# Optimization experiments

Measured on AMD Instinct MI355X. Metric: run time of the kernel, lower is better.

Reference implementation:

```python
import jax, jax.numpy as jnp
import numpy as np

SCALAR_DIM = 452          # 2 + 6 + (110+1)*4
GRID_C, GRID_H, GRID_W = 2, 32, 18
GRID_FLAT = GRID_C * GRID_H * GRID_W  # 1152
OBS_DIM = SCALAR_DIM + GRID_FLAT      # 1604
CNN_OUT, SC_OUT, HID, N_ACT = 128, 64, 128, 2305
CNN_FLAT = 64 * 8 * 5                 # 32x18 -> 16x9 -> 8x5
T, B = 256, 128


def setup_inputs() -> dict:
    key = jax.random.key(0)
    ks = jax.random.split(key, 24)
    p = lambda k, shape: jax.random.normal(k, shape, jnp.float32) * 0.02
    return dict(
        obs_seq=jax.random.uniform(ks[0], (T, B, OBS_DIM), jnp.float32),
        h0=jnp.zeros((1, B, HID), jnp.float32),
        c0=jnp.zeros((1, B, HID), jnp.float32),
        done_mask=jax.random.randint(ks[1], (T, B), 0, 2) > 0,
        conv1_w=p(ks[2], (32, GRID_C, 3, 3)), conv1_b=jnp.zeros((32,), jnp.float32),
        conv2_w=p(ks[3], (64, 32, 3, 3)),     conv2_b=jnp.zeros((64,), jnp.float32),
        conv3_w=p(ks[4], (64, 64, 3, 3)),     conv3_b=jnp.zeros((64,), jnp.float32),
        fc_w=p(ks[5], (CNN_OUT, CNN_FLAT)),   fc_b=jnp.zeros((CNN_OUT,), jnp.float32),
        s1_w=p(ks[6], (64, SCALAR_DIM)),      s1_b=jnp.zeros((64,), jnp.float32),
        s2_w=p(ks[7], (SC_OUT, 64)),          s2_b=jnp.zeros((SC_OUT,), jnp.float32),
        w_ih=p(ks[8], (4 * HID, CNN_OUT + SC_OUT)),
        w_hh=p(ks[9], (4 * HID, HID)),
        b_ih=jnp.zeros((4 * HID,), jnp.float32),
        b_hh=jnp.zeros((4 * HID,), jnp.float32),
        pol_w=p(ks[10], (N_ACT, HID)), pol_b=jnp.zeros((N_ACT,), jnp.float32),
        val_w=p(ks[11], (1, HID)),     val_b=jnp.zeros((1,), jnp.float32),
    )


def _conv(x, w, b, stride):
    y = jax.lax.conv_general_dilated(
        x, w, (stride, stride), ((1, 1), (1, 1)),
        dimension_numbers=("NCHW", "OIHW", "NCHW"))
    return y + b[None, :, None, None]


def reference(obs_seq, h0, c0, done_mask,
              conv1_w, conv1_b, conv2_w, conv2_b, conv3_w, conv3_b,
              fc_w, fc_b, s1_w, s1_b, s2_w, s2_b,
              w_ih, w_hh, b_ih, b_hh, pol_w, pol_b, val_w, val_b):
    Tt, Bb, _ = obs_seq.shape
    flat = obs_seq.reshape(Tt * Bb, -1)
    scalars = flat[:, :SCALAR_DIM]
    grid = flat[:, SCALAR_DIM:SCALAR_DIM + GRID_FLAT].reshape(-1, GRID_C, GRID_H, GRID_W)

    # CNN encoder
    x = jax.nn.relu(_conv(grid, conv1_w, conv1_b, 1))
    x = jax.nn.relu(_conv(x, conv2_w, conv2_b, 2))
    x = jax.nn.relu(_conv(x, conv3_w, conv3_b, 2))
    cnn = jax.nn.relu(x.reshape(x.shape[0], -1) @ fc_w.T + fc_b)

    # scalar MLP
    sc = jax.nn.relu(jax.nn.relu(scalars @ s1_w.T + s1_b) @ s2_w.T + s2_b)

    emb = jnp.concatenate([cnn, sc], axis=-1).reshape(Tt, Bb, -1)  # (T,B,192)

    # episode-reset mask applied BEFORE each step (for t>0, from done[t-1])
    keep = jnp.concatenate(
        [jnp.ones((1, Bb), jnp.float32),
         1.0 - done_mask[:-1].astype(jnp.float32)], axis=0)[..., None]  # (T,B,1)

    def step(carry, inp):
        h, c = carry
        x_t, k_t = inp
        h = h * k_t
        c = c * k_t
        g = x_t @ w_ih.T + h @ w_hh.T + b_ih + b_hh
        i, f, gg, o = jnp.split(g, 4, axis=-1)  # torch gate order i,f,g,o
        c = jax.nn.sigmoid(f) * c + jax.nn.sigmoid(i) * jnp.tanh(gg)
        h = jax.nn.sigmoid(o) * jnp.tanh(c)
        return (h, c), h

    (h_f, c_f), outs = jax.lax.scan(step, (h0[0], c0[0]), (emb, keep))

    logits = outs @ pol_w.T + pol_b   # (T,B,n_actions)
    values = outs @ val_w.T + val_b   # (T,B,1)
    return logits, values, h_f[None], c_f[None]
```

## Files before the change

kernel.cpp:

```cpp
#include <hip/hip_runtime.h>


typedef __attribute__((ext_vector_type(8))) short v8s;
typedef __attribute__((ext_vector_type(4))) float v4f;
typedef __attribute__((ext_vector_type(4))) unsigned int v4u;

#define DEV static __device__ __forceinline__

DEV unsigned int cvtpk(float lo, float hi){
  unsigned int d;
  asm("v_cvt_pk_bf16_f32 %0, %1, %2" : "=v"(d) : "v"(lo), "v"(hi));
  return d;
}
DEV unsigned short f2bf(float x){ return (unsigned short)(cvtpk(x, x) & 0xffffu); }
DEV float bf2f(unsigned short h){ return __uint_as_float(((unsigned int)h) << 16); }
DEV unsigned int pkbf(float a, float b){ return cvtpk(a, b); }
DEV v4f MFMA(v8s a, v8s b, v4f c){ return __builtin_amdgcn_mfma_f32_16x16x32_bf16(a, b, c, 0, 0, 0); }
DEV v4f vzero(){ v4f z = {0.f, 0.f, 0.f, 0.f}; return z; }
DEV float relu(float x){ return x > 0.f ? x : 0.f; }
DEV float sigm(float x){ return 1.0f / (1.0f + __expf(-x)); }
DEV float tanhfast(float x){
  x = fminf(15.0f, fmaxf(-15.0f, x));
  float e = __expf(2.0f * x);
  return (e - 1.0f) / (e + 1.0f);
}
DEV uint2 pack4(v4f a, float4 b){
  return make_uint2(cvtpk(relu(a[0]+b.x), relu(a[1]+b.y)),
                    cvtpk(relu(a[2]+b.z), relu(a[3]+b.w)));
}
union U8S { v4u u4; v8s s8; };

__global__ __launch_bounds__(256) void pack_all(
    const float* __restrict__ c1w, const float* __restrict__ c2w,
    const float* __restrict__ c3w, const float* __restrict__ fcw,
    const float* __restrict__ s1w, const float* __restrict__ s2w,
    const float* __restrict__ wih, const float* __restrict__ whh,
    const float* __restrict__ pw,
    unsigned short* __restrict__ w1p, unsigned short* __restrict__ w2p,
    unsigned short* __restrict__ w3p, unsigned short* __restrict__ fcp,
    unsigned short* __restrict__ s1p, unsigned short* __restrict__ s2p,
    unsigned short* __restrict__ lsp, unsigned short* __restrict__ pop){
  int b = blockIdx.x;
  const float *src, *src2 = nullptr; unsigned short* dst;
  int N, K, KS, CI, mode, rel;
  if      (b < 4)   { src=c1w; dst=w1p; N=32;  K=24;  KS=1;  CI=2;  mode=4; rel=b; }
  else if (b < 76)  { src=c2w; dst=w2p; N=64;  K=288; KS=9;  CI=32; mode=1; rel=b-4; }
  else if (b < 220) { src=c3w; dst=w3p; N=64;  K=576; KS=18; CI=64; mode=1; rel=b-76; }
  else if (b < 1500){ src=fcw; dst=fcp; N=128; K=2560;KS=80; CI=0;  mode=2; rel=b-220; }
  else if (b < 1620){ src=s1w; dst=s1p; N=64;  K=452; KS=15; CI=0;  mode=0; rel=b-1500; }
  else if (b < 1636){ src=s2w; dst=s2p; N=64;  K=64;  KS=2;  CI=0;  mode=0; rel=b-1620; }
  else if (b < 2276){ src=wih; src2=whh; dst=lsp; N=512; K=320; KS=10; CI=0; mode=3; rel=b-1636; }
  else              { src=pw;  dst=pop; N=2305;K=128; KS=4;  CI=0;  mode=0; rel=b-2276; }
  int idx = rel * 256 + threadIdx.x;
  int e  = idx & 7;
  int l  = (idx >> 3) & 63;
  int fs = idx >> 9;
  int ks = fs % KS;
  int nt = fs / KS;
  int n = nt * 16 + (l & 15);
  int k = ks * 32 + (l >> 4) * 8 + e;
  float v = 0.f;
  if (n < N && k < K){
    if (mode == 0)      v = src[n * K + k];
    else if (mode == 1){ int p9 = k / CI, ci = k - p9 * CI; v = src[(n * CI + ci) * 9 + p9]; }
    else if (mode == 2){ int pos = k >> 6, ci = k & 63;     v = src[n * 2560 + ci * 40 + pos]; }
    else if (mode == 3) v = (k < 192) ? src[n * 192 + k] : src2[n * 128 + (k - 192)];
    else { int dy = k >> 3, r = k & 7, dx = r >> 1, ci = r & 1;
           if (dx < 3) v = src[(n * 2 + ci) * 9 + dy * 3 + dx]; }
  }
  dst[idx] = f2bf(v);
}

__global__ __launch_bounds__(512) void bias_kernel(const float* __restrict__ bih,
    const float* __restrict__ bhh, float* __restrict__ bias512){
  int t = threadIdx.x;
  if (t < 512) bias512[t] = bih[t] + bhh[t];
}

__global__ __launch_bounds__(256) void mlp_kernel(const float* __restrict__ obs,
    const unsigned short* __restrict__ s1p, const unsigned short* __restrict__ s2p,
    const float* __restrict__ s1b, const float* __restrict__ s2b,
    unsigned short* __restrict__ emb){
  __shared__ __align__(16) unsigned short xl[32 * 488];
  __shared__ __align__(16) unsigned short h1[32 * 72];
  int tid = threadIdx.x, w = tid >> 6, l = tid & 63, i = l & 15, u = l >> 4;
  long s0 = (long)blockIdx.x * 32;
  for (int idx = tid; idx < 32 * 113; idx += 256){
    int r = idx / 113, q = idx - r * 113;
    float4 v = *(const float4*)&obs[(s0 + r) * 1604 + q * 4];
    *(uint2*)&xl[r * 488 + q * 4] = make_uint2(pkbf(v.x, v.y), pkbf(v.z, v.w));
  }
  for (int idx = tid; idx < 32 * 28; idx += 256){
    int r = idx / 28, k = 452 + (idx - r * 28);
    xl[r * 488 + k] = 0;
  }
  __syncthreads();
  v4f acc0 = vzero(), acc1 = vzero();
  const v8s* F1 = (const v8s*)s1p;
  #pragma unroll
  for (int ks = 0; ks < 15; ++ks){
    v8s bb = F1[(w * 15 + ks) * 64 + l];
    v8s aa0 = *(const v8s*)&xl[(0 * 16 + i) * 488 + ks * 32 + u * 8];
    v8s aa1 = *(const v8s*)&xl[(1 * 16 + i) * 488 + ks * 32 + u * 8];
    acc0 = MFMA(aa0, bb, acc0);
    acc1 = MFMA(aa1, bb, acc1);
  }
  float b1 = s1b[w * 16 + i];
  #pragma unroll
  for (int r = 0; r < 4; ++r){
    float v0 = relu(acc0[r] + b1);
    float v1 = relu(acc1[r] + b1);
    h1[(u * 4 + r) * 72 + w * 16 + i] = f2bf(v0);
    h1[(16 + u * 4 + r) * 72 + w * 16 + i] = f2bf(v1);
  }
  __syncthreads();
  v4f a20 = vzero(), a21 = vzero();
  const v8s* F2 = (const v8s*)s2p;
  #pragma unroll
  for (int ks = 0; ks < 2; ++ks){
    v8s bb = F2[(w * 2 + ks) * 64 + l];
    v8s aa0 = *(const v8s*)&h1[(0 * 16 + i) * 72 + ks * 32 + u * 8];
    v8s aa1 = *(const v8s*)&h1[(1 * 16 + i) * 72 + ks * 32 + u * 8];
    a20 = MFMA(aa0, bb, a20);
    a21 = MFMA(aa1, bb, a21);
  }
  float b2 = s2b[w * 16 + i];
  #pragma unroll
  for (int r = 0; r < 4; ++r){
    float v0 = relu(a20[r] + b2);
    float v1 = relu(a21[r] + b2);
    emb[(s0 + u * 4 + r) * 192 + 128 + w * 16 + i] = f2bf(v0);
    emb[(s0 + 16 + u * 4 + r) * 192 + 128 + w * 16 + i] = f2bf(v1);
  }
}

#define ACT1o 0
#define ACT2o 43520
#define GRIDo 68864
#define SWZ(p) ((((p) >> 1) & 7) << 4)

__global__ __launch_bounds__(512, 2) void conv_kernel(const float* __restrict__ obs,
    const unsigned short* __restrict__ w1p, const unsigned short* __restrict__ w2p,
    const unsigned short* __restrict__ w3p,
    const float* __restrict__ b1v, const float* __restrict__ b2v, const float* __restrict__ b3v,
    unsigned short* __restrict__ act3g){
  __shared__ __align__(16) char lds[74496];
  int tid = threadIdx.x, w = tid >> 6, l = tid & 63, i = l & 15, u = l >> 4;
  int nh2 = w & 1, pt2 = w >> 1;
  int cp = w & 1, t3 = w >> 1;
  const v8s* W1 = (const v8s*)w1p;
  const v8s* W2 = (const v8s*)w2p;
  const v8s* W3 = (const v8s*)w3p;
  v8s w1f0 = W1[l], w1f1 = W1[64 + l];
  float4 bc1a = *(const float4*)&b1v[u * 4];
  float4 bc1b = *(const float4*)&b1v[16 + u * 4];
  float4 bc2a = *(const float4*)&b2v[nh2 * 32 + u * 4];
  float4 bc2b = *(const float4*)&b2v[nh2 * 32 + 16 + u * 4];
  float4 bc3a = *(const float4*)&b3v[cp * 32 + u * 4];
  float4 bc3b = *(const float4*)&b3v[cp * 32 + 16 + u * 4];
  for (int idx = tid; idx < 18624; idx += 512) *(unsigned int*)(lds + idx * 4) = 0u;
  int soff[4];
  #pragma unroll
  for (int j = 0; j < 4; ++j){
    int p = tid * 4 + j, r = p / 18, c = p - r * 18;
    soff[j] = ((r + 1) * 20 + (c + 1)) * 4;
  }
  __syncthreads();
  long sbase = (long)blockIdx.x * 64;
  if (tid < 144){
    const float4* gp = (const float4*)(obs + sbase * 1604 + 452);
    float4 a = gp[tid], b = gp[tid + 144];
    *(unsigned int*)(lds + GRIDo + soff[0]) = pkbf(a.x, b.x);
    *(unsigned int*)(lds + GRIDo + soff[1]) = pkbf(a.y, b.y);
    *(unsigned int*)(lds + GRIDo + soff[2]) = pkbf(a.z, b.z);
    *(unsigned int*)(lds + GRIDo + soff[3]) = pkbf(a.w, b.w);
  }
  __syncthreads();

  int praw3 = t3 * 16 + i;
  int pos3 = praw3 > 39 ? 39 : praw3;
  int oh3 = pos3 / 5, ow3 = pos3 - oh3 * 5;
  int pr3 = (2 * oh3) * 11 + 2 * ow3;

  for (int it = 0; it < 64; ++it){
    long s = sbase + it;
    int gbo = GRIDo + (it & 1) * 2816;
    int z2; asm("s_mov_b32 %0, 0" : "=s"(z2) : "s"(it));
    v8s w2f[2][9];
    #pragma unroll
    for (int jj = 0; jj < 2; ++jj)
      #pragma unroll
      for (int t = 0; t < 9; ++t) w2f[jj][t] = W2[((nh2 * 2 + jj) * 9 + t) * 64 + l + z2];
    float4 pa, pb; bool pf = (it < 63) && (tid < 144);
    if (pf){
      const float4* gp = (const float4*)(obs + (s + 1) * 1604 + 452);
      pa = gp[tid]; pb = gp[tid + 144];
    }
    #pragma unroll
    for (int k = 0; k < 5; ++k){
      int ntl = w + 8 * k;
      if (ntl < 36){
        int pos = ntl * 16 + i;
        int oh = pos / 18, ow = pos - oh * 18;
        int glin = gbo + ((oh + u) * 20 + ow) * 4;
        U8S gv;
        gv.u4.x = *(const unsigned int*)(lds + glin);
        gv.u4.y = *(const unsigned int*)(lds + glin + 4);
        gv.u4.z = *(const unsigned int*)(lds + glin + 8);
        gv.u4.w = *(const unsigned int*)(lds + glin + 12);
        v4f a0 = MFMA(w1f0, gv.s8, vzero());
        v4f a1 = MFMA(w1f1, gv.s8, vzero());
        int p1 = (oh + 1) * 20 + (ow + 1);
        int sA = SWZ(p1);
        *(uint2*)(lds + ACT1o + ((p1 * 64 + u * 8) ^ sA))      = pack4(a0, bc1a);
        *(uint2*)(lds + ACT1o + ((p1 * 64 + 32 + u * 8) ^ sA)) = pack4(a1, bc1b);
      }
    }
    __syncthreads();
    #pragma unroll
    for (int kk = 0; kk < 3; ++kk){
      int ntl = pt2 + 4 * kk;
      if (ntl < 9){
        int pos2 = ntl * 16 + i;
        int oh = pos2 / 9, ow = pos2 - oh * 9;
        int pr0 = (2 * oh) * 20 + 2 * ow;
        v4f a0 = vzero(), a1 = vzero();
        #pragma unroll
        for (int dy = 0; dy < 3; ++dy)
          #pragma unroll
          for (int dx = 0; dx < 3; ++dx){
            int p = pr0 + dy * 20 + dx;
            int byte = (p * 64 + u * 16) ^ SWZ(p);
            v8s bf = *(const v8s*)(lds + ACT1o + byte);
            a0 = MFMA(w2f[0][dy * 3 + dx], bf, a0);
            a1 = MFMA(w2f[1][dy * 3 + dx], bf, a1);
          }
        int p2 = (oh + 1) * 11 + (ow + 1);
        int sB = SWZ(p2);
        *(uint2*)(lds + ACT2o + ((p2 * 128 + nh2 * 64 + u * 8) ^ sB))      = pack4(a0, bc2a);
        *(uint2*)(lds + ACT2o + ((p2 * 128 + nh2 * 64 + 32 + u * 8) ^ sB)) = pack4(a1, bc2b);
      }
    }
    if (pf){
      int gbn = GRIDo + ((it + 1) & 1) * 2816;
      *(unsigned int*)(lds + gbn + soff[0]) = pkbf(pa.x, pb.x);
      *(unsigned int*)(lds + gbn + soff[1]) = pkbf(pa.y, pb.y);
      *(unsigned int*)(lds + gbn + soff[2]) = pkbf(pa.z, pb.z);
      *(unsigned int*)(lds + gbn + soff[3]) = pkbf(pa.w, pb.w);
    }
    __syncthreads();
    if (w < 6){
      int z3; asm("s_mov_b32 %0, 0" : "=s"(z3) : "s"(it));
      v4f c30 = vzero(), c31 = vzero();
      #pragma unroll
      for (int ksh = 0; ksh < 2; ++ksh){
        const int t0 = ksh * 5, tc = ksh ? 4 : 5;
        v8s w3q[2][5][2];
        #pragma unroll
        for (int j = 0; j < 2; ++j)
          #pragma unroll
          for (int tt = 0; tt < 5; ++tt){
            if (tt < tc){
              #pragma unroll
              for (int h = 0; h < 2; ++h)
                w3q[j][tt][h] = W3[((2 * cp + j) * 18 + 2 * (t0 + tt) + h) * 64 + l + z3];
            }
          }
        #pragma unroll
        for (int tt = 0; tt < 5; ++tt){
          if (tt < tc){
            int tap = t0 + tt, dy = tap / 3, dx = tap - dy * 3;
            int dpp = dy * 11 + dx;
            #pragma unroll
            for (int h = 0; h < 2; ++h){
              int p = pr3 + dpp;
              int byte = (p * 128 + h * 64 + u * 16) ^ SWZ(p);
              v8s bf = *(const v8s*)(lds + ACT2o + byte);
              c30 = MFMA(w3q[0][tt][h], bf, c30);
              c31 = MFMA(w3q[1][tt][h], bf, c31);
            }
          }
        }
      }
      if (praw3 < 40){
        unsigned short* dg = act3g + s * 2560;
        *(uint2*)(dg + praw3 * 64 + cp * 32 + u * 4)      = pack4(c30, bc3a);
        *(uint2*)(dg + praw3 * 64 + cp * 32 + 16 + u * 4) = pack4(c31, bc3b);
      }
    }
  }
}

__global__ __launch_bounds__(256) void fc_kernel(const unsigned short* __restrict__ act3g,
    const unsigned short* __restrict__ fcp, const float* __restrict__ fcb,
    unsigned short* __restrict__ emb){
  __shared__ __align__(16) unsigned short al[64 * 264];
  int tid = threadIdx.x, w = tid >> 6, l = tid & 63, i = l & 15, u = l >> 4;
  long s0 = (long)blockIdx.x * 64;
  v4f acc[4][2];
  #pragma unroll
  for (int mt = 0; mt < 4; ++mt){ acc[mt][0] = vzero(); acc[mt][1] = vzero(); }
  const v8s* F = (const v8s*)fcp;
  for (int kc = 0; kc < 10; ++kc){
    __syncthreads();
    for (int idx = tid; idx < 64 * 32; idx += 256){
      int r = idx >> 5, q = idx & 31;
      *(v8s*)&al[r * 264 + q * 8] = *(const v8s*)&act3g[(s0 + r) * 2560 + kc * 256 + q * 8];
    }
    __syncthreads();
    #pragma unroll
    for (int ksl = 0; ksl < 8; ++ksl){
      v8s b0 = F[((w * 2 + 0) * 80 + kc * 8 + ksl) * 64 + l];
      v8s b1 = F[((w * 2 + 1) * 80 + kc * 8 + ksl) * 64 + l];
      #pragma unroll
      for (int mt = 0; mt < 4; ++mt){
        v8s aa = *(const v8s*)&al[(mt * 16 + i) * 264 + ksl * 32 + u * 8];
        acc[mt][0] = MFMA(aa, b0, acc[mt][0]);
        acc[mt][1] = MFMA(aa, b1, acc[mt][1]);
      }
    }
  }
  float fb0 = fcb[(w * 2) * 16 + i], fb1 = fcb[(w * 2 + 1) * 16 + i];
  #pragma unroll
  for (int mt = 0; mt < 4; ++mt)
    #pragma unroll
    for (int r = 0; r < 4; ++r){
      float v0 = relu(acc[mt][0][r] + fb0);
      float v1 = relu(acc[mt][1][r] + fb1);
      emb[(s0 + mt * 16 + u * 4 + r) * 192 + (w * 2) * 16 + i] = f2bf(v0);
      emb[(s0 + mt * 16 + u * 4 + r) * 192 + (w * 2 + 1) * 16 + i] = f2bf(v1);
    }
}

__global__ __launch_bounds__(256) void segprep_kernel(const void* __restrict__ dmask,
    unsigned int* __restrict__ segs, int4* __restrict__ gtab, int* __restrict__ meta){
  __shared__ int cnt[257], off[257], place[257];
  __shared__ int notInt;
  int tid = threadIdx.x;
  for (int idx = tid; idx < 257; idx += 256){ cnt[idx] = 0; place[idx] = 0; }
  if (tid == 0) notInt = 0;
  __syncthreads();
  const unsigned char* p8 = (const unsigned char*)dmask;
  int nz = 0;
  for (int idx = tid; idx < 2048; idx += 256)
    if (p8[idx * 4 + 1] | p8[idx * 4 + 2] | p8[idx * 4 + 3]) nz = 1;
  if (nz) notInt = 1;
  __syncthreads();
  bool m32 = (notInt == 0);
  const int* p32 = (const int*)dmask;
  if (tid < 128){
    int b = tid, ts = 0;
    for (int t = 0; t < 256; ++t){
      bool d = (t == 255) ? true : (m32 ? (p32[t * 128 + b] != 0) : (p8[t * 128 + b] != 0));
      if (d){ atomicAdd(&cnt[t - ts + 1], 1); ts = t + 1; }
    }
  }
  __syncthreads();
  if (tid == 0){
    int acc = 0;
    for (int len = 1; len <= 256; ++len){ off[len] = acc; acc += cnt[len]; }
    int G = 0;
    for (int len = 1; len <= 256; ++len){
      int c = cnt[len], g = 0;
      while (c > 0){
        int take = c < 32 ? c : 32;
        gtab[G] = make_int4(len, off[len] + g * 32, take, 0);
        ++G; c -= 32; ++g;
      }
    }
    meta[0] = G;
  }
  __syncthreads();
  if (tid < 128){
    int b = tid, ts = 0;
    for (int t = 0; t < 256; ++t){
      bool d = (t == 255) ? true : (m32 ? (p32[t * 128 + b] != 0) : (p8[t * 128 + b] != 0));
      if (d){
        int len = t - ts + 1;
        int slot = off[len] + atomicAdd(&place[len], 1);
        segs[slot] = (unsigned int)(b | (ts << 8));
        ts = t + 1;
      }
    }
  }
}

__global__ __launch_bounds__(512) void lstm_kernel(
    const unsigned short* __restrict__ emb, const unsigned short* __restrict__ lstmp,
    const float* __restrict__ bias512,
    const float* __restrict__ h0, const float* __restrict__ c0,
    const unsigned int* __restrict__ segs, const int4* __restrict__ gtab,
    const int* __restrict__ meta,
    unsigned short* __restrict__ outsb, float* __restrict__ hf, float* __restrict__ cf){
  int grp = blockIdx.x;
  if (grp >= meta[0]) return;
  int4 gd = gtab[grp];
  int len = gd.x, base = gd.y, nseg = gd.z;
  __shared__ __align__(16) unsigned short hbuf[2][32 * 136];
  __shared__ int sb[32], st[32];
  int tid = threadIdx.x, w = tid >> 6, l = tid & 63, i = l & 15, u = l >> 4;
  if (tid < 32){
    unsigned int sv = segs[base + (tid < nseg ? tid : 0)];
    sb[tid] = (int)(sv & 127u);
    st[tid] = (int)((sv >> 8) & 255u);
  }
  __syncthreads();
  int j = w * 16 + i;
  float cst[2][4];
  #pragma unroll
  for (int mt = 0; mt < 2; ++mt)
    #pragma unroll
    for (int r = 0; r < 4; ++r){
      int slot = mt * 16 + u * 4 + r;
      float cv = 0.f, hv = 0.f;
      if (st[slot] == 0){ cv = c0[sb[slot] * 128 + j]; hv = h0[sb[slot] * 128 + j]; }
      cst[mt][r] = cv;
      hbuf[0][slot * 136 + j] = f2bf(hv);
    }
  float bi = bias512[j], bff = bias512[128 + j], bg = bias512[256 + j], bo = bias512[384 + j];
  int bA0 = sb[i], tA0 = st[i];
  int bA1 = sb[16 + i], tA1 = st[16 + i];
  __syncthreads();
  const v8s* LP = (const v8s*)lstmp;
  for (int step = 0; step < len; ++step){
    int pb = step & 1;
    v4f gi0 = vzero(), gi1 = vzero(), gf0 = vzero(), gf1 = vzero();
    v4f gg0 = vzero(), gg1 = vzero(), go0 = vzero(), go1 = vzero();
    #pragma unroll
    for (int ks = 0; ks < 10; ++ks){
      v8s a0, a1;
      if (ks < 6){
        a0 = *(const v8s*)&emb[((long)(tA0 + step) * 128 + bA0) * 192 + ks * 32 + u * 8];
        a1 = *(const v8s*)&emb[((long)(tA1 + step) * 128 + bA1) * 192 + ks * 32 + u * 8];
      } else {
        int koff = (ks - 6) * 32 + u * 8;
        a0 = *(const v8s*)&hbuf[pb][i * 136 + koff];
        a1 = *(const v8s*)&hbuf[pb][(16 + i) * 136 + koff];
      }
      v8s b_i = LP[((w) * 10 + ks) * 64 + l];
      v8s b_f = LP[((w + 8) * 10 + ks) * 64 + l];
      v8s b_g = LP[((w + 16) * 10 + ks) * 64 + l];
      v8s b_o = LP[((w + 24) * 10 + ks) * 64 + l];
      gi0 = MFMA(a0, b_i, gi0); gi1 = MFMA(a1, b_i, gi1);
      gf0 = MFMA(a0, b_f, gf0); gf1 = MFMA(a1, b_f, gf1);
      gg0 = MFMA(a0, b_g, gg0); gg1 = MFMA(a1, b_g, gg1);
      go0 = MFMA(a0, b_o, go0); go1 = MFMA(a1, b_o, go1);
    }
    #pragma unroll
    for (int mt = 0; mt < 2; ++mt)
      #pragma unroll
      for (int r = 0; r < 4; ++r){
        int slot = mt * 16 + u * 4 + r;
        float giv = mt ? gi1[r] : gi0[r];
        float gfv = mt ? gf1[r] : gf0[r];
        float ggv = mt ? gg1[r] : gg0[r];
        float gov = mt ? go1[r] : go0[r];
        float iv = sigm(giv + bi);
        float fv = sigm(gfv + bff);
        float gv = tanhfast(ggv + bg);
        float ov = sigm(gov + bo);
        float cv = fv * cst[mt][r] + iv * gv;
        cst[mt][r] = cv;
        float hv = ov * tanhfast(cv);
        unsigned short hb = f2bf(hv);
        hbuf[pb ^ 1][slot * 136 + j] = hb;
        if (slot < nseg){
          outsb[((long)(st[slot] + step) * 128 + sb[slot]) * 128 + j] = hb;
          if (st[slot] + len == 256 && step == len - 1){
            hf[sb[slot] * 128 + j] = hv;
            cf[sb[slot] * 128 + j] = cv;
          }
        }
      }
    __syncthreads();
  }
}

__global__ __launch_bounds__(256) void heads_kernel(const unsigned short* __restrict__ outsb,
    const unsigned short* __restrict__ polp, const float* __restrict__ polb,
    const float* __restrict__ vw, const float* __restrict__ vb,
    float* __restrict__ logits, float* __restrict__ values){
  __shared__ __align__(16) unsigned short al[64 * 136];
  int tid = threadIdx.x, w = tid >> 6, l = tid & 63, i = l & 15, u = l >> 4;
  long s0 = (long)blockIdx.x * 64;
  for (int idx = tid; idx < 64 * 16; idx += 256){
    int r = idx >> 4, q = idx & 15;
    *(v8s*)&al[r * 136 + q * 8] = *(const v8s*)&outsb[(s0 + r) * 128 + q * 8];
  }
  __syncthreads();
  v8s af[4][4];
  #pragma unroll
  for (int mt = 0; mt < 4; ++mt)
    #pragma unroll
    for (int ks = 0; ks < 4; ++ks)
      af[mt][ks] = *(const v8s*)&al[(mt * 16 + i) * 136 + ks * 32 + u * 8];
  const v8s* P = (const v8s*)polp;
  for (int nt = w; nt < 145; nt += 4){
    v4f acc[4];
    #pragma unroll
    for (int mt = 0; mt < 4; ++mt) acc[mt] = vzero();
    #pragma unroll
    for (int ks = 0; ks < 4; ++ks){
      v8s bb = P[(nt * 4 + ks) * 64 + l];
      #pragma unroll
      for (int mt = 0; mt < 4; ++mt) acc[mt] = MFMA(af[mt][ks], bb, acc[mt]);
    }
    int n = nt * 16 + i;
    if (n < 2305){
      float pbv = polb[n];
      #pragma unroll
      for (int mt = 0; mt < 4; ++mt)
        #pragma unroll
        for (int r = 0; r < 4; ++r)
          logits[(s0 + mt * 16 + u * 4 + r) * 2305 + n] = acc[mt][r] + pbv;
    }
  }
  float vacc = 0.f;
  #pragma unroll
  for (int g = 0; g < 4; ++g){
    float4 vA = *(const float4*)&vw[g * 32 + u * 8];
    float4 vB = *(const float4*)&vw[g * 32 + u * 8 + 4];
    v8s xv = *(const v8s*)&al[(w * 16 + i) * 136 + g * 32 + u * 8];
    vacc += bf2f((unsigned short)xv[0]) * vA.x + bf2f((unsigned short)xv[1]) * vA.y
          + bf2f((unsigned short)xv[2]) * vA.z + bf2f((unsigned short)xv[3]) * vA.w
          + bf2f((unsigned short)xv[4]) * vB.x + bf2f((unsigned short)xv[5]) * vB.y
          + bf2f((unsigned short)xv[6]) * vB.z + bf2f((unsigned short)xv[7]) * vB.w;
  }
  vacc += __shfl_xor(vacc, 16);
  vacc += __shfl_xor(vacc, 32);
  if (u == 0) values[s0 + w * 16 + i] = vacc + vb[0];
}

extern "C" void kernel_launch(void* const* d_in, const int* in_sizes, int n_in,
                              void* d_out, int out_size, void* d_ws, size_t ws_size,
                              hipStream_t stream){
  (void)in_sizes; (void)n_in; (void)out_size; (void)ws_size;
  const float* obs = (const float*)d_in[0];
  const float* h0  = (const float*)d_in[1];
  const float* c0  = (const float*)d_in[2];
  const void*  dm  = d_in[3];
  const float* c1w = (const float*)d_in[4];  const float* c1b = (const float*)d_in[5];
  const float* c2w = (const float*)d_in[6];  const float* c2b = (const float*)d_in[7];
  const float* c3w = (const float*)d_in[8];  const float* c3b = (const float*)d_in[9];
  const float* fcw = (const float*)d_in[10]; const float* fcb = (const float*)d_in[11];
  const float* s1w = (const float*)d_in[12]; const float* s1b = (const float*)d_in[13];
  const float* s2w = (const float*)d_in[14]; const float* s2b = (const float*)d_in[15];
  const float* wih = (const float*)d_in[16]; const float* whh = (const float*)d_in[17];
  const float* bih = (const float*)d_in[18]; const float* bhh = (const float*)d_in[19];
  const float* pw  = (const float*)d_in[20]; const float* pb  = (const float*)d_in[21];
  const float* vw  = (const float*)d_in[22]; const float* vb  = (const float*)d_in[23];

  char* ws = (char*)d_ws;
  size_t off = 0;
  auto take = [&](size_t sz)->char*{
    char* p = ws + off; off = (off + sz + 255) & ~(size_t)255; return p;
  };
  unsigned short* emb    = (unsigned short*)take(32768UL * 192 * 2);
  unsigned short* outsb  = (unsigned short*)take(32768UL * 128 * 2);
  unsigned short* w1p    = (unsigned short*)take(1024UL * 2);
  unsigned short* w2p    = (unsigned short*)take(18432UL * 2);
  unsigned short* w3p    = (unsigned short*)take(36864UL * 2);
  unsigned short* fcp    = (unsigned short*)take(327680UL * 2);
  unsigned short* s1p    = (unsigned short*)take(30720UL * 2);
  unsigned short* s2p    = (unsigned short*)take(4096UL * 2);
  unsigned short* lsp    = (unsigned short*)take(163840UL * 2);
  unsigned short* pop    = (unsigned short*)take(296960UL * 2);
  float*          b512   = (float*)take(512UL * 4);
  unsigned int*   segs   = (unsigned int*)take(32768UL * 4);
  int4*           gtab   = (int4*)take(1280UL * 16);
  int*            meta   = (int*)take(256);

  float* outp   = (float*)d_out;
  float* logits = outp;
  float* values = outp + 75530240L;
  float* hf     = outp + 75563008L;
  float* cf     = outp + 75579392L;
  unsigned short* act3g = (unsigned short*)d_out;

  dim3 b256(256), b512t(512);
  pack_all<<<dim3(3436), b256, 0, stream>>>(c1w, c2w, c3w, fcw, s1w, s2w, wih, whh, pw,
                                            w1p, w2p, w3p, fcp, s1p, s2p, lsp, pop);
  bias_kernel<<<dim3(1), b512t, 0, stream>>>(bih, bhh, b512);
  segprep_kernel<<<dim3(1), b256, 0, stream>>>(dm, segs, gtab, meta);
  mlp_kernel<<<dim3(1024), b256, 0, stream>>>(obs, s1p, s2p, s1b, s2b, emb);
  conv_kernel<<<dim3(512), b512t, 0, stream>>>(obs, w1p, w2p, w3p, c1b, c2b, c3b, act3g);
  fc_kernel<<<dim3(512), b256, 0, stream>>>(act3g, fcp, fcb, emb);
  lstm_kernel<<<dim3(1280), b512t, 0, stream>>>(emb, lsp, b512, h0, c0, segs, gtab, meta,
                                                outsb, hf, cf);
  heads_kernel<<<dim3(512), b256, 0, stream>>>(outsb, pop, pb, vw, vb, logits, values);
}
```

Measured before the change: 1.209 ms.

## Repartition conv2/conv3 work so each wave owns one 16-channel tile

Conv2 and conv3 waves are remapped so each wave handles a single 16-output-channel tile across several position tiles, instead of two channel tiles over fewer positions. All 8 waves now take part in conv3, where before only 6 did; waves 0-3 also pick up the partial third position tile. Each wave loads half as many weight fragments into registers, which eases register pressure. The cost is more LDS reads of activations per MFMA, since each B fragment now feeds one MFMA rather than two, and the conv3 load is uneven across waves.

```diff
diff --git a/kernel.cpp b/kernel.cpp
--- a/kernel.cpp
+++ b/kernel.cpp
@@ -146,18 +146,16 @@
     unsigned short* __restrict__ act3g){
   __shared__ __align__(16) char lds[74496];
   int tid = threadIdx.x, w = tid >> 6, l = tid & 63, i = l & 15, u = l >> 4;
-  int nh2 = w & 1, pt2 = w >> 1;
-  int cp = w & 1, t3 = w >> 1;
+  int ct = w & 3;
+  int ph = w >> 2;
   const v8s* W1 = (const v8s*)w1p;
   const v8s* W2 = (const v8s*)w2p;
   const v8s* W3 = (const v8s*)w3p;
   v8s w1f0 = W1[l], w1f1 = W1[64 + l];
   float4 bc1a = *(const float4*)&b1v[u * 4];
   float4 bc1b = *(const float4*)&b1v[16 + u * 4];
-  float4 bc2a = *(const float4*)&b2v[nh2 * 32 + u * 4];
-  float4 bc2b = *(const float4*)&b2v[nh2 * 32 + 16 + u * 4];
-  float4 bc3a = *(const float4*)&b3v[cp * 32 + u * 4];
-  float4 bc3b = *(const float4*)&b3v[cp * 32 + 16 + u * 4];
+  float4 bc2  = *(const float4*)&b2v[ct * 16 + u * 4];
+  float4 bc3  = *(const float4*)&b3v[ct * 16 + u * 4];
   for (int idx = tid; idx < 18624; idx += 512) *(unsigned int*)(lds + idx * 4) = 0u;
   int soff[4];
   #pragma unroll
@@ -177,20 +175,22 @@
   }
   __syncthreads();
 
-  int praw3 = t3 * 16 + i;
-  int pos3 = praw3 > 39 ? 39 : praw3;
-  int oh3 = pos3 / 5, ow3 = pos3 - oh3 * 5;
+  int praw3 = ph * 16 + i;
+  int oh3 = praw3 / 5, ow3 = praw3 - oh3 * 5;
   int pr3 = (2 * oh3) * 11 + 2 * ow3;
+  int praw3s = 32 + i;
+  int pos3s = praw3s > 39 ? 39 : praw3s;
+  int oh3s = pos3s / 5, ow3s = pos3s - oh3s * 5;
+  int pr3s = (2 * oh3s) * 11 + 2 * ow3s;
+  bool small3 = (w < 4);
 
   for (int it = 0; it < 64; ++it){
     long s = sbase + it;
     int gbo = GRIDo + (it & 1) * 2816;
     int z2; asm("s_mov_b32 %0, 0" : "=s"(z2) : "s"(it));
-    v8s w2f[2][9];
-    #pragma unroll
-    for (int jj = 0; jj < 2; ++jj)
-      #pragma unroll
-      for (int t = 0; t < 9; ++t) w2f[jj][t] = W2[((nh2 * 2 + jj) * 9 + t) * 64 + l + z2];
+    v8s w2f[9];
+    #pragma unroll
+    for (int t = 0; t < 9; ++t) w2f[t] = W2[(ct * 9 + t) * 64 + l + z2];
     float4 pa, pb; bool pf = (it < 63) && (tid < 144);
     if (pf){
       const float4* gp = (const float4*)(obs + (s + 1) * 1604 + 452);
@@ -218,13 +218,13 @@
     }
     __syncthreads();
     #pragma unroll
-    for (int kk = 0; kk < 3; ++kk){
-      int ntl = pt2 + 4 * kk;
+    for (int kk = 0; kk < 5; ++kk){
+      int ntl = ph + 2 * kk;
       if (ntl < 9){
         int pos2 = ntl * 16 + i;
         int oh = pos2 / 9, ow = pos2 - oh * 9;
         int pr0 = (2 * oh) * 20 + 2 * ow;
-        v4f a0 = vzero(), a1 = vzero();
+        v4f a = vzero();
         #pragma unroll
         for (int dy = 0; dy < 3; ++dy)
           #pragma unroll
@@ -232,13 +232,10 @@
             int p = pr0 + dy * 20 + dx;
             int byte = (p * 64 + u * 16) ^ SWZ(p);
             v8s bf = *(const v8s*)(lds + ACT1o + byte);
-            a0 = MFMA(w2f[0][dy * 3 + dx], bf, a0);
-            a1 = MFMA(w2f[1][dy * 3 + dx], bf, a1);
+            a = MFMA(w2f[dy * 3 + dx], bf, a);
           }
         int p2 = (oh + 1) * 11 + (ow + 1);
-        int sB = SWZ(p2);
-        *(uint2*)(lds + ACT2o + ((p2 * 128 + nh2 * 64 + u * 8) ^ sB))      = pack4(a0, bc2a);
-        *(uint2*)(lds + ACT2o + ((p2 * 128 + nh2 * 64 + 32 + u * 8) ^ sB)) = pack4(a1, bc2b);
+        *(uint2*)(lds + ACT2o + ((p2 * 128 + ct * 32 + u * 8) ^ SWZ(p2))) = pack4(a, bc2);
       }
     }
     if (pf){
@@ -249,44 +246,37 @@
       *(unsigned int*)(lds + gbn + soff[3]) = pkbf(pa.w, pb.w);
     }
     __syncthreads();
-    if (w < 6){
+    {
       int z3; asm("s_mov_b32 %0, 0" : "=s"(z3) : "s"(it));
-      v4f c30 = vzero(), c31 = vzero();
+      v4f c3 = vzero(), c3s = vzero();
       #pragma unroll
       for (int ksh = 0; ksh < 2; ++ksh){
-        const int t0 = ksh * 5, tc = ksh ? 4 : 5;
-        v8s w3q[2][5][2];
+        v8s w3h[9];
         #pragma unroll
-        for (int j = 0; j < 2; ++j)
-          #pragma unroll
-          for (int tt = 0; tt < 5; ++tt){
-            if (tt < tc){
-              #pragma unroll
-              for (int h = 0; h < 2; ++h)
-                w3q[j][tt][h] = W3[((2 * cp + j) * 18 + 2 * (t0 + tt) + h) * 64 + l + z3];
-            }
+        for (int t = 0; t < 9; ++t) w3h[t] = W3[(ct * 18 + ksh * 9 + t) * 64 + l + z3];
+        #pragma unroll
+        for (int t = 0; t < 9; ++t){
+          int ks = ksh * 9 + t, tap = ks >> 1, h = ks & 1;
+          int dy = tap / 3, dx = tap - dy * 3;
+          int dpp = dy * 11 + dx;
+          {
+            int p = pr3 + dpp;
+            int byte = (p * 128 + h * 64 + u * 16) ^ SWZ(p);
+            v8s bf = *(const v8s*)(lds + ACT2o + byte);
+            c3 = MFMA(w3h[t], bf, c3);
           }
-        #pragma unroll
-        for (int tt = 0; tt < 5; ++tt){
-          if (tt < tc){
-            int tap = t0 + tt, dy = tap / 3, dx = tap - dy * 3;
-            int dpp = dy * 11 + dx;
-            #pragma unroll
-            for (int h = 0; h < 2; ++h){
-              int p = pr3 + dpp;
-              int byte = (p * 128 + h * 64 + u * 16) ^ SWZ(p);
-              v8s bf = *(const v8s*)(lds + ACT2o + byte);
-              c30 = MFMA(w3q[0][tt][h], bf, c30);
-              c31 = MFMA(w3q[1][tt][h], bf, c31);
-            }
+          if (small3){
+            int p = pr3s + dpp;
+            int byte = (p * 128 + h * 64 + u * 16) ^ SWZ(p);
+            v8s bf = *(const v8s*)(lds + ACT2o + byte);
+            c3s = MFMA(w3h[t], bf, c3s);
           }
         }
       }
-      if (praw3 < 40){
-        unsigned short* dg = act3g + s * 2560;
-        *(uint2*)(dg + praw3 * 64 + cp * 32 + u * 4)      = pack4(c30, bc3a);
-        *(uint2*)(dg + praw3 * 64 + cp * 32 + 16 + u * 4) = pack4(c31, bc3b);
-      }
+      unsigned short* dg = act3g + s * 2560;
+      *(uint2*)(dg + praw3 * 64 + ct * 16 + u * 4) = pack4(c3, bc3);
+      if (small3 && praw3s < 40)
+        *(uint2*)(dg + praw3s * 64 + ct * 16 + u * 4) = pack4(c3s, bc3);
     }
   }
 }
```

After: 1.172 ms (median of 3 runs). -3.0%, faster.

## Split conv1/conv2 into two row halves to shrink LDS and raise occupancy

Applied to the files above, without the earlier changes.

The conv kernel now computes conv1 and conv2 in two row-halves per sample, so the conv1 activation buffer only holds half the image (with halo rows). This cuts LDS from about 74KB to 52KB and lets blocks drop to 256 threads with three blocks per CU. Grid size doubles to 1024 blocks of 32 samples each. Work is redistributed over 4 waves, and conv3 gives each wave up to two position tiles. The cost is extra barriers per sample, recomputation of halo rows, and fewer waves per block.

```diff
diff --git a/kernel.cpp b/kernel.cpp
--- a/kernel.cpp
+++ b/kernel.cpp
@@ -135,30 +135,29 @@
 }
 
 #define ACT1o 0
-#define ACT2o 43520
-#define GRIDo 68864
+#define ACT2o 21760
+#define GRIDo 47104
 #define SWZ(p) ((((p) >> 1) & 7) << 4)
 
-__global__ __launch_bounds__(512, 2) void conv_kernel(const float* __restrict__ obs,
+__global__ __launch_bounds__(256, 3) void conv_kernel(const float* __restrict__ obs,
     const unsigned short* __restrict__ w1p, const unsigned short* __restrict__ w2p,
     const unsigned short* __restrict__ w3p,
     const float* __restrict__ b1v, const float* __restrict__ b2v, const float* __restrict__ b3v,
     unsigned short* __restrict__ act3g){
-  __shared__ __align__(16) char lds[74496];
+  __shared__ __align__(16) char lds[52736];
   int tid = threadIdx.x, w = tid >> 6, l = tid & 63, i = l & 15, u = l >> 4;
-  int nh2 = w & 1, pt2 = w >> 1;
-  int cp = w & 1, t3 = w >> 1;
+  int nh = w & 1, mh = w >> 1;
   const v8s* W1 = (const v8s*)w1p;
   const v8s* W2 = (const v8s*)w2p;
   const v8s* W3 = (const v8s*)w3p;
   v8s w1f0 = W1[l], w1f1 = W1[64 + l];
   float4 bc1a = *(const float4*)&b1v[u * 4];
   float4 bc1b = *(const float4*)&b1v[16 + u * 4];
-  float4 bc2a = *(const float4*)&b2v[nh2 * 32 + u * 4];
-  float4 bc2b = *(const float4*)&b2v[nh2 * 32 + 16 + u * 4];
-  float4 bc3a = *(const float4*)&b3v[cp * 32 + u * 4];
-  float4 bc3b = *(const float4*)&b3v[cp * 32 + 16 + u * 4];
-  for (int idx = tid; idx < 18624; idx += 512) *(unsigned int*)(lds + idx * 4) = 0u;
+  float4 bc2a = *(const float4*)&b2v[nh * 32 + u * 4];
+  float4 bc2b = *(const float4*)&b2v[nh * 32 + 16 + u * 4];
+  float4 bc3a = *(const float4*)&b3v[nh * 32 + u * 4];
+  float4 bc3b = *(const float4*)&b3v[nh * 32 + 16 + u * 4];
+  for (int idx = tid; idx < 13184; idx += 256) *(unsigned int*)(lds + idx * 4) = 0u;
   int soff[4];
   #pragma unroll
   for (int j = 0; j < 4; ++j){
@@ -166,7 +165,7 @@
     soff[j] = ((r + 1) * 20 + (c + 1)) * 4;
   }
   __syncthreads();
-  long sbase = (long)blockIdx.x * 64;
+  long sbase = (long)blockIdx.x * 32;
   if (tid < 144){
     const float4* gp = (const float4*)(obs + sbase * 1604 + 452);
     float4 a = gp[tid], b = gp[tid + 144];
@@ -177,12 +176,15 @@
   }
   __syncthreads();
 
-  int praw3 = t3 * 16 + i;
-  int pos3 = praw3 > 39 ? 39 : praw3;
-  int oh3 = pos3 / 5, ow3 = pos3 - oh3 * 5;
-  int pr3 = (2 * oh3) * 11 + 2 * ow3;
-
-  for (int it = 0; it < 64; ++it){
+  int pos3_0 = (mh ? 1 : 0) * 16 + i;
+  int pos3_1r = 32 + i;
+  int pos3_1 = pos3_1r > 39 ? 39 : pos3_1r;
+  int oh30 = pos3_0 / 5, ow30 = pos3_0 - oh30 * 5;
+  int oh31 = pos3_1 / 5, ow31 = pos3_1 - oh31 * 5;
+  int pr3_0 = (2 * oh30) * 11 + 2 * ow30;
+  int pr3_1 = (2 * oh31) * 11 + 2 * ow31;
+
+  for (int it = 0; it < 32; ++it){
     long s = sbase + it;
     int gbo = GRIDo + (it & 1) * 2816;
     int z2; asm("s_mov_b32 %0, 0" : "=s"(z2) : "s"(it));
@@ -190,68 +192,79 @@
     #pragma unroll
     for (int jj = 0; jj < 2; ++jj)
       #pragma unroll
-      for (int t = 0; t < 9; ++t) w2f[jj][t] = W2[((nh2 * 2 + jj) * 9 + t) * 64 + l + z2];
-    float4 pa, pb; bool pf = (it < 63) && (tid < 144);
+      for (int t = 0; t < 9; ++t) w2f[jj][t] = W2[((nh * 2 + jj) * 9 + t) * 64 + l + z2];
+    float4 pa, pb; bool pf = (it < 31) && (tid < 144);
     if (pf){
       const float4* gp = (const float4*)(obs + (s + 1) * 1604 + 452);
       pa = gp[tid]; pb = gp[tid + 144];
     }
     #pragma unroll
-    for (int k = 0; k < 5; ++k){
-      int ntl = w + 8 * k;
-      if (ntl < 36){
-        int pos = ntl * 16 + i;
-        int oh = pos / 18, ow = pos - oh * 18;
-        int glin = gbo + ((oh + u) * 20 + ow) * 4;
-        U8S gv;
-        gv.u4.x = *(const unsigned int*)(lds + glin);
-        gv.u4.y = *(const unsigned int*)(lds + glin + 4);
-        gv.u4.z = *(const unsigned int*)(lds + glin + 8);
-        gv.u4.w = *(const unsigned int*)(lds + glin + 12);
-        v4f a0 = MFMA(w1f0, gv.s8, vzero());
-        v4f a1 = MFMA(w1f1, gv.s8, vzero());
-        int p1 = (oh + 1) * 20 + (ow + 1);
-        int sA = SWZ(p1);
-        *(uint2*)(lds + ACT1o + ((p1 * 64 + u * 8) ^ sA))      = pack4(a0, bc1a);
-        *(uint2*)(lds + ACT1o + ((p1 * 64 + 32 + u * 8) ^ sA)) = pack4(a1, bc1b);
-      }
-    }
-    __syncthreads();
-    #pragma unroll
-    for (int kk = 0; kk < 3; ++kk){
-      int ntl = pt2 + 4 * kk;
-      if (ntl < 9){
-        int pos2 = ntl * 16 + i;
-        int oh = pos2 / 9, ow = pos2 - oh * 9;
-        int pr0 = (2 * oh) * 20 + 2 * ow;
-        v4f a0 = vzero(), a1 = vzero();
-        #pragma unroll
-        for (int dy = 0; dy < 3; ++dy)
+    for (int h = 0; h < 2; ++h){
+      if (h == 0 && tid < 160){
+        unsigned int* z = (unsigned int*)(lds + ACT1o);
+        z[tid] = 0u; z[tid + 160] = 0u;
+      }
+      int ntiles = h ? 20 : 18;
+      int maxpos = h ? 305 : 287;
+      int rbase  = h ? 15 : 0;
+      #pragma unroll
+      for (int k = 0; k < 5; ++k){
+        int ntl = w + 4 * k;
+        if (ntl < ntiles){
+          int pos = ntl * 16 + i; pos = pos > maxpos ? maxpos : pos;
+          int ohl = pos / 18, ow = pos - ohl * 18;
+          int glin = gbo + ((rbase + ohl + u) * 20 + ow) * 4;
+          U8S gv;
+          gv.u4.x = *(const unsigned int*)(lds + glin);
+          gv.u4.y = *(const unsigned int*)(lds + glin + 4);
+          gv.u4.z = *(const unsigned int*)(lds + glin + 8);
+          gv.u4.w = *(const unsigned int*)(lds + glin + 12);
+          v4f a0 = MFMA(w1f0, gv.s8, vzero());
+          v4f a1 = MFMA(w1f1, gv.s8, vzero());
+          int rb = h ? ohl : (ohl + 1);
+          int p1 = rb * 20 + (ow + 1);
+          int sA = SWZ(p1);
+          *(uint2*)(lds + ACT1o + ((p1 * 64 + u * 8) ^ sA))      = pack4(a0, bc1a);
+          *(uint2*)(lds + ACT1o + ((p1 * 64 + 32 + u * 8) ^ sA)) = pack4(a1, bc1b);
+        }
+      }
+      __syncthreads();
+      #pragma unroll
+      for (int k = 0; k < 3; ++k){
+        int ntl = mh + 2 * k;
+        if (ntl < 5){
+          int pos2 = ntl * 16 + i; pos2 = pos2 > 71 ? 71 : pos2;
+          int rl = pos2 / 9, ow = pos2 - rl * 9;
+          int pr0 = (2 * rl) * 20 + 2 * ow;
+          v4f a0 = vzero(), a1 = vzero();
           #pragma unroll
-          for (int dx = 0; dx < 3; ++dx){
-            int p = pr0 + dy * 20 + dx;
-            int byte = (p * 64 + u * 16) ^ SWZ(p);
-            v8s bf = *(const v8s*)(lds + ACT1o + byte);
-            a0 = MFMA(w2f[0][dy * 3 + dx], bf, a0);
-            a1 = MFMA(w2f[1][dy * 3 + dx], bf, a1);
-          }
-        int p2 = (oh + 1) * 11 + (ow + 1);
-        int sB = SWZ(p2);
-        *(uint2*)(lds + ACT2o + ((p2 * 128 + nh2 * 64 + u * 8) ^ sB))      = pack4(a0, bc2a);
-        *(uint2*)(lds + ACT2o + ((p2 * 128 + nh2 * 64 + 32 + u * 8) ^ sB)) = pack4(a1, bc2b);
-      }
-    }
-    if (pf){
-      int gbn = GRIDo + ((it + 1) & 1) * 2816;
-      *(unsigned int*)(lds + gbn + soff[0]) = pkbf(pa.x, pb.x);
-      *(unsigned int*)(lds + gbn + soff[1]) = pkbf(pa.y, pb.y);
-      *(unsigned int*)(lds + gbn + soff[2]) = pkbf(pa.z, pb.z);
-      *(unsigned int*)(lds + gbn + soff[3]) = pkbf(pa.w, pb.w);
-    }
-    __syncthreads();
-    if (w < 6){
+          for (int dy = 0; dy < 3; ++dy)
+            #pragma unroll
+            for (int dx = 0; dx < 3; ++dx){
+              int p = pr0 + dy * 20 + dx;
+              int byte = (p * 64 + u * 16) ^ SWZ(p);
+              v8s bf = *(const v8s*)(lds + ACT1o + byte);
+              a0 = MFMA(w2f[0][dy * 3 + dx], bf, a0);
+              a1 = MFMA(w2f[1][dy * 3 + dx], bf, a1);
+            }
+          int p2 = (8 * h + rl + 1) * 11 + (ow + 1);
+          int sB = SWZ(p2);
+          *(uint2*)(lds + ACT2o + ((p2 * 128 + nh * 64 + u * 8) ^ sB))      = pack4(a0, bc2a);
+          *(uint2*)(lds + ACT2o + ((p2 * 128 + nh * 64 + 32 + u * 8) ^ sB)) = pack4(a1, bc2b);
+        }
+      }
+      if (h == 1 && pf){
+        int gbn = GRIDo + ((it + 1) & 1) * 2816;
+        *(unsigned int*)(lds + gbn + soff[0]) = pkbf(pa.x, pb.x);
+        *(unsigned int*)(lds + gbn + soff[1]) = pkbf(pa.y, pb.y);
+        *(unsigned int*)(lds + gbn + soff[2]) = pkbf(pa.z, pb.z);
+        *(unsigned int*)(lds + gbn + soff[3]) = pkbf(pa.w, pb.w);
+      }
+      __syncthreads();
+    }
+    {
       int z3; asm("s_mov_b32 %0, 0" : "=s"(z3) : "s"(it));
-      v4f c30 = vzero(), c31 = vzero();
+      v4f c300 = vzero(), c301 = vzero(), c310 = vzero(), c311 = vzero();
       #pragma unroll
       for (int ksh = 0; ksh < 2; ++ksh){
         const int t0 = ksh * 5, tc = ksh ? 4 : 5;
@@ -262,8 +275,8 @@
           for (int tt = 0; tt < 5; ++tt){
             if (tt < tc){
               #pragma unroll
-              for (int h = 0; h < 2; ++h)
-                w3q[j][tt][h] = W3[((2 * cp + j) * 18 + 2 * (t0 + tt) + h) * 64 + l + z3];
+              for (int h2 = 0; h2 < 2; ++h2)
+                w3q[j][tt][h2] = W3[((2 * nh + j) * 18 + 2 * (t0 + tt) + h2) * 64 + l + z3];
             }
           }
         #pragma unroll
@@ -272,20 +285,31 @@
             int tap = t0 + tt, dy = tap / 3, dx = tap - dy * 3;
             int dpp = dy * 11 + dx;
             #pragma unroll
-            for (int h = 0; h < 2; ++h){
-              int p = pr3 + dpp;
-              int byte = (p * 128 + h * 64 + u * 16) ^ SWZ(p);
-              v8s bf = *(const v8s*)(lds + ACT2o + byte);
-              c30 = MFMA(w3q[0][tt][h], bf, c30);
-              c31 = MFMA(w3q[1][tt][h], bf, c31);
+            for (int h2 = 0; h2 < 2; ++h2){
+              {
+                int p = pr3_0 + dpp;
+                int byte = (p * 128 + h2 * 64 + u * 16) ^ SWZ(p);
+                v8s bf = *(const v8s*)(lds + ACT2o + byte);
+                c300 = MFMA(w3q[0][tt][h2], bf, c300);
+                c301 = MFMA(w3q[1][tt][h2], bf, c301);
+              }
+              if (mh == 0){
+                int p = pr3_1 + dpp;
+                int byte = (p * 128 + h2 * 64 + u * 16) ^ SWZ(p);
+                v8s bf = *(const v8s*)(lds + ACT2o + byte);
+                c310 = MFMA(w3q[0][tt][h2], bf, c310);
+                c311 = MFMA(w3q[1][tt][h2], bf, c311);
+              }
             }
           }
         }
       }
-      if (praw3 < 40){
-        unsigned short* dg = act3g + s * 2560;
-        *(uint2*)(dg + praw3 * 64 + cp * 32 + u * 4)      = pack4(c30, bc3a);
-        *(uint2*)(dg + praw3 * 64 + cp * 32 + 16 + u * 4) = pack4(c31, bc3b);
+      unsigned short* dg = act3g + s * 2560;
+      *(uint2*)(dg + pos3_0 * 64 + nh * 32 + u * 4)      = pack4(c300, bc3a);
+      *(uint2*)(dg + pos3_0 * 64 + nh * 32 + 16 + u * 4) = pack4(c301, bc3b);
+      if (mh == 0 && pos3_1r < 40){
+        *(uint2*)(dg + pos3_1r * 64 + nh * 32 + u * 4)      = pack4(c310, bc3a);
+        *(uint2*)(dg + pos3_1r * 64 + nh * 32 + 16 + u * 4) = pack4(c311, bc3b);
       }
     }
   }
@@ -583,7 +607,7 @@
   bias_kernel<<<dim3(1), b512t, 0, stream>>>(bih, bhh, b512);
   segprep_kernel<<<dim3(1), b256, 0, stream>>>(dm, segs, gtab, meta);
   mlp_kernel<<<dim3(1024), b256, 0, stream>>>(obs, s1p, s2p, s1b, s2b, emb);
-  conv_kernel<<<dim3(512), b512t, 0, stream>>>(obs, w1p, w2p, w3p, c1b, c2b, c3b, act3g);
+  conv_kernel<<<dim3(1024), b256, 0, stream>>>(obs, w1p, w2p, w3p, c1b, c2b, c3b, act3g);
   fc_kernel<<<dim3(512), b256, 0, stream>>>(act3g, fcp, fcb, emb);
   lstm_kernel<<<dim3(1280), b512t, 0, stream>>>(emb, lsp, b512, h0, c0, segs, gtab, meta,
                                                 outsb, hf, cf);
```

After: 2.250 ms. +86.1%, slower.

## Shrink conv kernel to four waves and redistribute per-wave conv work

Applied to the files above, without the earlier changes.

The conv kernel now runs with 256 threads per block instead of 512. The conv1, conv2 and conv3 tile assignments are remapped over four waves. In conv3, waves with mh==0 each handle two output-position tiles, reusing the same loaded weight fragments. The aim is to cut idle waves and barrier cost, since the old layout had only 6 of 8 waves active in conv3 and uneven conv1 tiles. In exchange, each wave carries more serial work and fewer waves per CU are left to hide LDS and MFMA latency.

```diff
diff --git a/kernel.cpp b/kernel.cpp
--- a/kernel.cpp
+++ b/kernel.cpp
@@ -139,26 +139,25 @@
 #define GRIDo 68864
 #define SWZ(p) ((((p) >> 1) & 7) << 4)
 
-__global__ __launch_bounds__(512, 2) void conv_kernel(const float* __restrict__ obs,
+__global__ __launch_bounds__(256, 2) void conv_kernel(const float* __restrict__ obs,
     const unsigned short* __restrict__ w1p, const unsigned short* __restrict__ w2p,
     const unsigned short* __restrict__ w3p,
     const float* __restrict__ b1v, const float* __restrict__ b2v, const float* __restrict__ b3v,
     unsigned short* __restrict__ act3g){
   __shared__ __align__(16) char lds[74496];
   int tid = threadIdx.x, w = tid >> 6, l = tid & 63, i = l & 15, u = l >> 4;
-  int nh2 = w & 1, pt2 = w >> 1;
-  int cp = w & 1, t3 = w >> 1;
+  int nh = w & 1, mh = w >> 1;
   const v8s* W1 = (const v8s*)w1p;
   const v8s* W2 = (const v8s*)w2p;
   const v8s* W3 = (const v8s*)w3p;
   v8s w1f0 = W1[l], w1f1 = W1[64 + l];
   float4 bc1a = *(const float4*)&b1v[u * 4];
   float4 bc1b = *(const float4*)&b1v[16 + u * 4];
-  float4 bc2a = *(const float4*)&b2v[nh2 * 32 + u * 4];
-  float4 bc2b = *(const float4*)&b2v[nh2 * 32 + 16 + u * 4];
-  float4 bc3a = *(const float4*)&b3v[cp * 32 + u * 4];
-  float4 bc3b = *(const float4*)&b3v[cp * 32 + 16 + u * 4];
-  for (int idx = tid; idx < 18624; idx += 512) *(unsigned int*)(lds + idx * 4) = 0u;
+  float4 bc2a = *(const float4*)&b2v[nh * 32 + u * 4];
+  float4 bc2b = *(const float4*)&b2v[nh * 32 + 16 + u * 4];
+  float4 bc3a = *(const float4*)&b3v[nh * 32 + u * 4];
+  float4 bc3b = *(const float4*)&b3v[nh * 32 + 16 + u * 4];
+  for (int idx = tid; idx < 18624; idx += 256) *(unsigned int*)(lds + idx * 4) = 0u;
   int soff[4];
   #pragma unroll
   for (int j = 0; j < 4; ++j){
@@ -177,10 +176,13 @@
   }
   __syncthreads();
 
-  int praw3 = t3 * 16 + i;
-  int pos3 = praw3 > 39 ? 39 : praw3;
-  int oh3 = pos3 / 5, ow3 = pos3 - oh3 * 5;
-  int pr3 = (2 * oh3) * 11 + 2 * ow3;
+  int pos3_0 = (mh ? 1 : 0) * 16 + i;
+  int pos3_1r = 32 + i;
+  int pos3_1 = pos3_1r > 39 ? 39 : pos3_1r;
+  int oh30 = pos3_0 / 5, ow30 = pos3_0 - oh30 * 5;
+  int oh31 = pos3_1 / 5, ow31 = pos3_1 - oh31 * 5;
+  int pr3_0 = (2 * oh30) * 11 + 2 * ow30;
+  int pr3_1 = (2 * oh31) * 11 + 2 * ow31;
 
   for (int it = 0; it < 64; ++it){
     long s = sbase + it;
@@ -190,56 +192,50 @@
     #pragma unroll
     for (int jj = 0; jj < 2; ++jj)
       #pragma unroll
-      for (int t = 0; t < 9; ++t) w2f[jj][t] = W2[((nh2 * 2 + jj) * 9 + t) * 64 + l + z2];
+      for (int t = 0; t < 9; ++t) w2f[jj][t] = W2[((nh * 2 + jj) * 9 + t) * 64 + l + z2];
     float4 pa, pb; bool pf = (it < 63) && (tid < 144);
     if (pf){
       const float4* gp = (const float4*)(obs + (s + 1) * 1604 + 452);
       pa = gp[tid]; pb = gp[tid + 144];
     }
     #pragma unroll
-    for (int k = 0; k < 5; ++k){
-      int ntl = w + 8 * k;
-      if (ntl < 36){
-        int pos = ntl * 16 + i;
-        int oh = pos / 18, ow = pos - oh * 18;
-        int glin = gbo + ((oh + u) * 20 + ow) * 4;
-        U8S gv;
-        gv.u4.x = *(const unsigned int*)(lds + glin);
-        gv.u4.y = *(const unsigned int*)(lds + glin + 4);
-        gv.u4.z = *(const unsigned int*)(lds + glin + 8);
-        gv.u4.w = *(const unsigned int*)(lds + glin + 12);
-        v4f a0 = MFMA(w1f0, gv.s8, vzero());
-        v4f a1 = MFMA(w1f1, gv.s8, vzero());
-        int p1 = (oh + 1) * 20 + (ow + 1);
-        int sA = SWZ(p1);
-        *(uint2*)(lds + ACT1o + ((p1 * 64 + u * 8) ^ sA))      = pack4(a0, bc1a);
-        *(uint2*)(lds + ACT1o + ((p1 * 64 + 32 + u * 8) ^ sA)) = pack4(a1, bc1b);
-      }
+    for (int k = 0; k < 9; ++k){
+      int ntl = w + 4 * k;
+      int pos = ntl * 16 + i;
+      int oh = pos / 18, ow = pos - oh * 18;
+      int glin = gbo + ((oh + u) * 20 + ow) * 4;
+      U8S gv;
+      gv.u4.x = *(const unsigned int*)(lds + glin);
+      gv.u4.y = *(const unsigned int*)(lds + glin + 4);
+      gv.u4.z = *(const unsigned int*)(lds + glin + 8);
+      gv.u4.w = *(const unsigned int*)(lds + glin + 12);
+      v4f a0 = MFMA(w1f0, gv.s8, vzero());
+      v4f a1 = MFMA(w1f1, gv.s8, vzero());
+      int p1 = (oh + 1) * 20 + (ow + 1);
+      int sA = SWZ(p1);
+      *(uint2*)(lds + ACT1o + ((p1 * 64 + u * 8) ^ sA))      = pack4(a0, bc1a);
+      *(uint2*)(lds + ACT1o + ((p1 * 64 + 32 + u * 8) ^ sA)) = pack4(a1, bc1b);
     }
     __syncthreads();
-    #pragma unroll
-    for (int kk = 0; kk < 3; ++kk){
-      int ntl = pt2 + 4 * kk;
-      if (ntl < 9){
-        int pos2 = ntl * 16 + i;
-        int oh = pos2 / 9, ow = pos2 - oh * 9;
-        int pr0 = (2 * oh) * 20 + 2 * ow;
-        v4f a0 = vzero(), a1 = vzero();
+    for (int ntl = mh; ntl < 9; ntl += 2){
+      int pos2 = ntl * 16 + i;
+      int oh = pos2 / 9, ow = pos2 - oh * 9;
+      int pr0 = (2 * oh) * 20 + 2 * ow;
+      v4f a0 = vzero(), a1 = vzero();
+      #pragma unroll
+      for (int dy = 0; dy < 3; ++dy)
         #pragma unroll
-        for (int dy = 0; dy < 3; ++dy)
-          #pragma unroll
-          for (int dx = 0; dx < 3; ++dx){
-            int p = pr0 + dy * 20 + dx;
-            int byte = (p * 64 + u * 16) ^ SWZ(p);
-            v8s bf = *(const v8s*)(lds + ACT1o + byte);
-            a0 = MFMA(w2f[0][dy * 3 + dx], bf, a0);
-            a1 = MFMA(w2f[1][dy * 3 + dx], bf, a1);
-          }
-        int p2 = (oh + 1) * 11 + (ow + 1);
-        int sB = SWZ(p2);
-        *(uint2*)(lds + ACT2o + ((p2 * 128 + nh2 * 64 + u * 8) ^ sB))      = pack4(a0, bc2a);
-        *(uint2*)(lds + ACT2o + ((p2 * 128 + nh2 * 64 + 32 + u * 8) ^ sB)) = pack4(a1, bc2b);
-      }
+        for (int dx = 0; dx < 3; ++dx){
+          int p = pr0 + dy * 20 + dx;
+          int byte = (p * 64 + u * 16) ^ SWZ(p);
+          v8s bf = *(const v8s*)(lds + ACT1o + byte);
+          a0 = MFMA(w2f[0][dy * 3 + dx], bf, a0);
+          a1 = MFMA(w2f[1][dy * 3 + dx], bf, a1);
+        }
+      int p2 = (oh + 1) * 11 + (ow + 1);
+      int sB = SWZ(p2);
+      *(uint2*)(lds + ACT2o + ((p2 * 128 + nh * 64 + u * 8) ^ sB))      = pack4(a0, bc2a);
+      *(uint2*)(lds + ACT2o + ((p2 * 128 + nh * 64 + 32 + u * 8) ^ sB)) = pack4(a1, bc2b);
     }
     if (pf){
       int gbn = GRIDo + ((it + 1) & 1) * 2816;
@@ -249,9 +245,9 @@
       *(unsigned int*)(lds + gbn + soff[3]) = pkbf(pa.w, pb.w);
     }
     __syncthreads();
-    if (w < 6){
+    {
       int z3; asm("s_mov_b32 %0, 0" : "=s"(z3) : "s"(it));
-      v4f c30 = vzero(), c31 = vzero();
+      v4f c300 = vzero(), c301 = vzero(), c310 = vzero(), c311 = vzero();
       #pragma unroll
       for (int ksh = 0; ksh < 2; ++ksh){
         const int t0 = ksh * 5, tc = ksh ? 4 : 5;
@@ -263,7 +259,7 @@
             if (tt < tc){
               #pragma unroll
               for (int h = 0; h < 2; ++h)
-                w3q[j][tt][h] = W3[((2 * cp + j) * 18 + 2 * (t0 + tt) + h) * 64 + l + z3];
+                w3q[j][tt][h] = W3[((2 * nh + j) * 18 + 2 * (t0 + tt) + h) * 64 + l + z3];
             }
           }
         #pragma unroll
@@ -273,19 +269,30 @@
             int dpp = dy * 11 + dx;
             #pragma unroll
             for (int h = 0; h < 2; ++h){
-              int p = pr3 + dpp;
-              int byte = (p * 128 + h * 64 + u * 16) ^ SWZ(p);
-              v8s bf = *(const v8s*)(lds + ACT2o + byte);
-              c30 = MFMA(w3q[0][tt][h], bf, c30);
-              c31 = MFMA(w3q[1][tt][h], bf, c31);
+              {
+                int p = pr3_0 + dpp;
+                int byte = (p * 128 + h * 64 + u * 16) ^ SWZ(p);
+                v8s bf = *(const v8s*)(lds + ACT2o + byte);
+                c300 = MFMA(w3q[0][tt][h], bf, c300);
+                c301 = MFMA(w3q[1][tt][h], bf, c301);
+              }
+              if (mh == 0){
+                int p = pr3_1 + dpp;
+                int byte = (p * 128 + h * 64 + u * 16) ^ SWZ(p);
+                v8s bf = *(const v8s*)(lds + ACT2o + byte);
+                c310 = MFMA(w3q[0][tt][h], bf, c310);
+                c311 = MFMA(w3q[1][tt][h], bf, c311);
+              }
             }
           }
         }
       }
-      if (praw3 < 40){
-        unsigned short* dg = act3g + s * 2560;
-        *(uint2*)(dg + praw3 * 64 + cp * 32 + u * 4)      = pack4(c30, bc3a);
-        *(uint2*)(dg + praw3 * 64 + cp * 32 + 16 + u * 4) = pack4(c31, bc3b);
+      unsigned short* dg = act3g + s * 2560;
+      *(uint2*)(dg + pos3_0 * 64 + nh * 32 + u * 4)      = pack4(c300, bc3a);
+      *(uint2*)(dg + pos3_0 * 64 + nh * 32 + 16 + u * 4) = pack4(c301, bc3b);
+      if (mh == 0 && pos3_1r < 40){
+        *(uint2*)(dg + pos3_1r * 64 + nh * 32 + u * 4)      = pack4(c310, bc3a);
+        *(uint2*)(dg + pos3_1r * 64 + nh * 32 + 16 + u * 4) = pack4(c311, bc3b);
       }
     }
   }
@@ -583,7 +590,7 @@
   bias_kernel<<<dim3(1), b512t, 0, stream>>>(bih, bhh, b512);
   segprep_kernel<<<dim3(1), b256, 0, stream>>>(dm, segs, gtab, meta);
   mlp_kernel<<<dim3(1024), b256, 0, stream>>>(obs, s1p, s2p, s1b, s2b, emb);
-  conv_kernel<<<dim3(512), b512t, 0, stream>>>(obs, w1p, w2p, w3p, c1b, c2b, c3b, act3g);
+  conv_kernel<<<dim3(512), b256, 0, stream>>>(obs, w1p, w2p, w3p, c1b, c2b, c3b, act3g);
   fc_kernel<<<dim3(512), b256, 0, stream>>>(act3g, fcp, fcb, emb);
   lstm_kernel<<<dim3(1280), b512t, 0, stream>>>(emb, lsp, b512, h0, c0, segs, gtab, meta,
                                                 outsb, hf, cf);
```

New measurement: 1.025 ms. 15.2% less time.
